# Kernel optimization log

Hardware: AMD Instinct MI355X
Metric: run time of the kernel (lower is better)

The kernel has to match this reference:

```python
import jax, jax.numpy as jnp
import numpy as np
from functools import partial

D_MODEL = 1024
D_HIDDEN = 4096
N_BLOCKS = 4
D_VOCAB = 32000
BATCH = 2
SEQ = 2048
LN_EPS = 1e-5
LRELU_SLOPE = 0.01  # torch nn.LeakyReLU default


def setup_inputs() -> dict:
    key = jax.random.key(0)
    ks = jax.random.split(key, 16)
    d, h, L, v = D_MODEL, D_HIDDEN, N_BLOCKS, D_VOCAB
    scale = d ** 0.5
    inp = {
        "tokens": jax.random.randint(ks[0], (BATCH, SEQ), 0, v, dtype=jnp.int64)
                  if jax.config.jax_enable_x64 else
                  jax.random.randint(ks[0], (BATCH, SEQ), 0, v, dtype=jnp.int32),
        "emb": jax.random.normal(ks[1], (v, d), jnp.float32) * 0.02,
        # per-block stacked params (leading axis = layer) for lax.scan
        "qk": jax.random.normal(ks[2], (L, d, d), jnp.float32) / scale,
        "ov": jax.random.normal(ks[3], (L, d, d), jnp.float32) / scale,
        "w_up": jax.random.normal(ks[4], (L, d, h), jnp.float32) / scale,
        "b_up": jnp.zeros((L, h), jnp.float32),
        "w_hid": jax.random.normal(ks[5], (L, h, h), jnp.float32) / (h ** 0.5),
        "b_hid": jnp.zeros((L, h), jnp.float32),
        "w_down": jax.random.normal(ks[6], (L, h, d), jnp.float32) / (h ** 0.5),
        "b_down": jnp.zeros((L, d), jnp.float32),
        "ln1_g": jnp.ones((L, d), jnp.float32),
        "ln1_b": jnp.zeros((L, d), jnp.float32),
        "ln2_g": jnp.ones((L, d), jnp.float32),
        "ln2_b": jnp.zeros((L, d), jnp.float32),
    }
    return inp


def _layer_norm(x, g, b):
    mu = jnp.mean(x, axis=-1, keepdims=True)
    var = jnp.mean(jnp.square(x - mu), axis=-1, keepdims=True)
    return (x - mu) * jax.lax.rsqrt(var + LN_EPS) * g + b


def _forward(tokens, emb, qk, ov, w_up, b_up, w_hid, b_hid, w_down, b_down,
             ln1_g, ln1_b, ln2_g, ln2_b):
    x = emb[tokens]                                   # [B, S, D]
    seq = tokens.shape[1]
    scale = jnp.asarray(D_MODEL ** 0.5, x.dtype)
    causal = jnp.tril(jnp.ones((seq, seq), bool))     # True = keep

    def block(x, p):
        (qk, ov, w_up, b_up, w_hid, b_hid, w_down, b_down,
         g1, b1, g2, b2) = p
        h = _layer_norm(x, g1, b1)
        # attention: (h @ qk @ h^T) / sqrt(d), causal mask, softmax, @ h @ ov
        scores = jnp.einsum('bsd,de,bte->bst', h, qk, h) / scale
        scores = jnp.where(causal, scores, -jnp.inf)
        attn = jax.nn.softmax(scores, axis=-1)
        x = x + jnp.einsum('bst,btd,de->bse', attn, h, ov)
        # MLP with LeakyReLU after every layer (incl. output)
        m = _layer_norm(x, g2, b2)
        m = jax.nn.leaky_relu(m @ w_up + b_up, LRELU_SLOPE)
        m = jax.nn.leaky_relu(m @ w_hid + b_hid, LRELU_SLOPE)
        m = jax.nn.leaky_relu(m @ w_down + b_down, LRELU_SLOPE)
        return x + m, None

    params = (qk, ov, w_up, b_up, w_hid, b_hid, w_down, b_down,
              ln1_g, ln1_b, ln2_g, ln2_b)
    x, _ = jax.lax.scan(block, x, params)
    return x @ emb.T                                  # [B, S, V] logits


@jax.jit
def reference(tokens, emb, qk, ov, w_up, b_up, w_hid, b_hid, w_down, b_down,
              ln1_g, ln1_b, ln2_g, ln2_b):
    return _forward(tokens, emb, qk, ov, w_up, b_up, w_hid, b_hid,
                    w_down, b_down, ln1_g, ln1_b, ln2_g, ln2_b)
```

## Files before the change

kernel.cpp:

```cpp
#include <hip/hip_runtime.h>

#define BS   4096
#define SEQL 2048
#define DM   1024
#define DH   4096
#define NV   32000

using u16 = unsigned short;

typedef __attribute__((ext_vector_type(8))) short bf16x8;
typedef __attribute__((ext_vector_type(4))) float f32x4;

__device__ __forceinline__ u16 f2b(float f) {
  union { float f; unsigned u; } c; c.f = f;
  unsigned u = c.u;
  u = (u + 0x7FFFu + ((u >> 16) & 1u)) >> 16;
  return (u16)u;
}

__device__ __forceinline__ void gld16(const u16* g, u16* l) {
  __builtin_amdgcn_global_load_lds(
      (__attribute__((address_space(1))) void*)(void*)const_cast<u16*>(g),
      (__attribute__((address_space(3))) void*)l, 16, 0, 0);
}

__global__ __launch_bounds__(256) void k_embed(const int* __restrict__ tok,
                                               const float* __restrict__ emb,
                                               float* __restrict__ x) {
  const long row = blockIdx.x;
  const long e = tok[row];
  ((float4*)(x + row * DM))[threadIdx.x] = ((const float4*)(emb + e * DM))[threadIdx.x];
}

__global__ __launch_bounds__(256) void k_cvt(const float* __restrict__ in,
                                             u16* __restrict__ out, int n4) {
  int i = blockIdx.x * 256 + threadIdx.x;
  if (i < n4) {
    float4 v = ((const float4*)in)[i];
    ushort4 o;
    o.x = f2b(v.x); o.y = f2b(v.y); o.z = f2b(v.z); o.w = f2b(v.w);
    ((ushort4*)out)[i] = o;
  }
}

__global__ __launch_bounds__(256) void k_ln(const float* __restrict__ x,
                                            const float* __restrict__ g,
                                            const float* __restrict__ b,
                                            u16* __restrict__ out) {
  const long row = blockIdx.x;
  const int t = threadIdx.x;
  float4 v = ((const float4*)(x + row * DM))[t];
  float s  = v.x + v.y + v.z + v.w;
  float q2 = v.x*v.x + v.y*v.y + v.z*v.z + v.w*v.w;
#pragma unroll
  for (int o = 1; o < 64; o <<= 1) { s += __shfl_xor(s, o); q2 += __shfl_xor(q2, o); }
  __shared__ float rs_[4], rq_[4];
  const int lane = t & 63, wid = t >> 6;
  if (lane == 0) { rs_[wid] = s; rq_[wid] = q2; }
  __syncthreads();
  s  = rs_[0] + rs_[1] + rs_[2] + rs_[3];
  q2 = rq_[0] + rq_[1] + rq_[2] + rq_[3];
  const float mu   = s * (1.f / 1024.f);
  const float var  = q2 * (1.f / 1024.f) - mu * mu;
  const float rstd = rsqrtf(var + 1e-5f);
  float4 gg = ((const float4*)g)[t];
  float4 bb = ((const float4*)b)[t];
  ushort4 o;
  o.x = f2b((v.x - mu) * rstd * gg.x + bb.x);
  o.y = f2b((v.y - mu) * rstd * gg.y + bb.y);
  o.z = f2b((v.z - mu) * rstd * gg.z + bb.z);
  o.w = f2b((v.w - mu) * rstd * gg.w + bb.w);
  ((ushort4*)(out + row * DM))[t] = o;
}

__device__ __forceinline__ u16 to_b16(float v) { return f2b(v); }
__device__ __forceinline__ u16 to_b16(u16 v)   { return v; }

template <typename T>
__global__ __launch_bounds__(256) void k_transpose64(const T* __restrict__ in,
                                                     u16* __restrict__ out,
                                                     int R, int C, long inz, long outz) {
  __shared__ u16 tile[64][65];
  const T* ip = in + (long)blockIdx.z * inz;
  u16* op = out + (long)blockIdx.z * outz;
  const int tx = threadIdx.x & 63, ty = threadIdx.x >> 6;
  const long c0 = (long)blockIdx.x * 64, r0 = (long)blockIdx.y * 64;
#pragma unroll
  for (int i = 0; i < 16; ++i)
    tile[ty + i * 4][tx] = to_b16(ip[(r0 + ty + i * 4) * C + c0 + tx]);
  __syncthreads();
#pragma unroll
  for (int i = 0; i < 16; ++i)
    op[(c0 + ty + i * 4) * R + r0 + tx] = tile[tx][ty + i * 4];
}

__global__ __launch_bounds__(256) void k_softmax(const float* __restrict__ sc,
                                                 u16* __restrict__ at) {
  const int r = blockIdx.x;
  const long z = blockIdx.y;
  const int t = threadIdx.x;
  const float* row = sc + (z * SEQL + r) * SEQL;
  u16* orow = at + (z * SEQL + r) * SEQL;
  const int ni = (r >> 8) + 1;
  float vals[8];
  float mx = -3.4e38f;
  for (int i = 0; i < ni; ++i) {
    int c = i * 256 + t;
    float v = (c <= r) ? row[c] : -3.4e38f;
    vals[i] = v;
    mx = fmaxf(mx, v);
  }
#pragma unroll
  for (int o = 1; o < 64; o <<= 1) mx = fmaxf(mx, __shfl_xor(mx, o));
  __shared__ float rm[4], rsum[4];
  const int lane = t & 63, wid = t >> 6;
  if (lane == 0) rm[wid] = mx;
  __syncthreads();
  mx = fmaxf(fmaxf(rm[0], rm[1]), fmaxf(rm[2], rm[3]));
  float sum = 0.f;
  for (int i = 0; i < ni; ++i) {
    int c = i * 256 + t;
    float e = (c <= r) ? __expf(vals[i] - mx) : 0.f;
    vals[i] = e;
    sum += e;
  }
#pragma unroll
  for (int o = 1; o < 64; o <<= 1) sum += __shfl_xor(sum, o);
  if (lane == 0) rsum[wid] = sum;
  __syncthreads();
  sum = rsum[0] + rsum[1] + rsum[2] + rsum[3];
  const float inv = 1.f / sum;
  for (int i = 0; i < ni; ++i) orow[i * 256 + t] = f2b(vals[i] * inv);
}

template <int EPI, bool BIAS, bool LRELU, int CAUSAL, bool XOUT>
__global__ __launch_bounds__(256, 2) void k_gemm_bt(
    const u16* __restrict__ A, const u16* __restrict__ B, void* __restrict__ C,
    const float* __restrict__ bias, u16* __restrict__ xb, int K, int N,
    long sAz, long sBz, long sCz, float scale) {
  __shared__ u16 lA[128 * 32];
  __shared__ u16 lB[128 * 32];
  const int t = threadIdx.x;
  const long z = blockIdx.z;
  const long row0 = (long)blockIdx.x * 128;
  const long col0 = (long)blockIdx.y * 128;
  if (CAUSAL == 1 && col0 > row0 + 127) return;
  const int Klim = (CAUSAL == 2) ? min(K, (int)row0 + 128) : K;
  const u16* Ab = A + z * sAz;
  const u16* Bb = B + z * sBz;

  const int rr = t >> 2;
  const int c8 = (t & 3) * 8;
  const u16* gA0 = Ab + (row0 + rr) * K + c8;
  const u16* gA1 = Ab + (row0 + 64 + rr) * K + c8;
  const u16* gB0 = Bb + (col0 + rr) * K + c8;
  const u16* gB1 = Bb + (col0 + 64 + rr) * K + c8;
  u16* sA0 = &lA[rr * 32 + c8];
  u16* sA1 = &lA[(64 + rr) * 32 + c8];
  u16* sB0 = &lB[rr * 32 + c8];
  u16* sB1 = &lB[(64 + rr) * 32 + c8];

  const int lane = t & 63;
  const int w = t >> 6;
  const int wr = (w >> 1) * 64, wc = (w & 1) * 64;
  const int fr = lane & 15;
  const int fk = (lane >> 4) * 8;

  f32x4 acc[4][4] = {};

  for (int k0 = 0; k0 < Klim; k0 += 32) {
    gld16(gA0 + k0, sA0);
    gld16(gA1 + k0, sA1);
    gld16(gB0 + k0, sB0);
    gld16(gB1 + k0, sB1);
    __syncthreads();
    bf16x8 av[4], bv[4];
#pragma unroll
    for (int m = 0; m < 4; ++m) av[m] = *(const bf16x8*)&lA[(wr + m * 16 + fr) * 32 + fk];
#pragma unroll
    for (int n = 0; n < 4; ++n) bv[n] = *(const bf16x8*)&lB[(wc + n * 16 + fr) * 32 + fk];
#pragma unroll
    for (int m = 0; m < 4; ++m)
#pragma unroll
      for (int n = 0; n < 4; ++n)
        acc[m][n] = __builtin_amdgcn_mfma_f32_16x16x32_bf16(av[m], bv[n], acc[m][n], 0, 0, 0);
    __syncthreads();
  }

  const int er = (lane >> 4) * 4;
  const int ec = lane & 15;
#pragma unroll
  for (int m = 0; m < 4; ++m) {
#pragma unroll
    for (int n = 0; n < 4; ++n) {
#pragma unroll
      for (int j = 0; j < 4; ++j) {
        long r = row0 + wr + m * 16 + er + j;
        long c = col0 + wc + n * 16 + ec;
        float v = acc[m][n][j] * scale;
        if (BIAS)  v += bias[c];
        if (LRELU) v = v > 0.f ? v : 0.01f * v;
        long idx = z * sCz + r * (long)N + c;
        if (EPI == 0)      ((float*)C)[idx] = v;
        else if (EPI == 1) ((u16*)C)[idx] = f2b(v);
        else {
          float nv = ((float*)C)[idx] + v;
          ((float*)C)[idx] = nv;
          if (XOUT) xb[idx] = f2b(nv);
        }
      }
    }
  }
}

template <int EPI, bool BIAS, bool LRELU, bool BAR2>
__device__ __forceinline__ void g256_body(
    u16* S, const u16* __restrict__ A, const u16* __restrict__ B,
    void* __restrict__ C, const float* __restrict__ bias, int K, int N, float scale) {
  char* Sc = (char*)S;
  const int t = threadIdx.x;
  const int lane = t & 63;
  const int w = t >> 6;
  const int wr = w >> 2;
  const int wc = w & 3;
  const long row0 = (long)blockIdx.x * 256;
  const long col0 = (long)blockIdx.y * 256;
  const int nt = K >> 6;

  int srow[2], scol[2], ldsb[2];
#pragma unroll
  for (int i = 0; i < 2; ++i) {
    int d = t * 16 + i * 8192;
    int dx = d ^ (((d >> 7) & 3) << 4);
    srow[i] = dx >> 6;
    scol[i] = (dx & 63) >> 1;
    ldsb[i] = d;
  }
  const u16* Abase = A + row0 * (long)K;
  const u16* Bbase = B + col0 * (long)K;

  auto stage = [&](int opb, int kh, int buf, int kb) {
#pragma unroll
    for (int i = 0; i < 2; ++i) {
      const u16* src = (opb ? Bbase : Abase) + (long)srow[i] * K + kb + kh * 32 + scol[i];
      u16* dst = &S[(buf * 4 + opb * 2 + kh) * 8192 + (ldsb[i] >> 1)];
      gld16(src, dst);
    }
  };

  const int fr = lane & 15;
  const int fky = lane >> 4;
  const int axor = ((fr >> 1) & 3) << 4;
  int aoff[8], boff[4];
#pragma unroll
  for (int m = 0; m < 8; ++m)
    aoff[m] = (((wr * 128 + m * 16 + fr) * 64) + fky * 16) ^ axor;
#pragma unroll
  for (int n = 0; n < 4; ++n)
    boff[n] = (((wc * 64 + n * 16 + fr) * 64) + fky * 16) ^ axor;

  f32x4 acc[8][4] = {};
  bf16x8 aA0, aA1, aA2, aA3, aB0, aB1, aB2, aB3;
  bf16x8 bX0, bX1, bX2, bX3, bY0, bY1, bY2, bY3;

#define RD_A(d0, d1, d2, d3, bb, kh, mh)                                   \
  { const char* Ah_ = Sc + (bb) * 65536 + (kh) * 16384;                    \
    d0 = *(const bf16x8*)(Ah_ + aoff[(mh) * 4 + 0]);                       \
    d1 = *(const bf16x8*)(Ah_ + aoff[(mh) * 4 + 1]);                       \
    d2 = *(const bf16x8*)(Ah_ + aoff[(mh) * 4 + 2]);                       \
    d3 = *(const bf16x8*)(Ah_ + aoff[(mh) * 4 + 3]); }
#define RD_B(d0, d1, d2, d3, bb, kh)                                       \
  { const char* Bh_ = Sc + (bb) * 65536 + 32768 + (kh) * 16384;            \
    d0 = *(const bf16x8*)(Bh_ + boff[0]);                                  \
    d1 = *(const bf16x8*)(Bh_ + boff[1]);                                  \
    d2 = *(const bf16x8*)(Bh_ + boff[2]);                                  \
    d3 = *(const bf16x8*)(Bh_ + boff[3]); }
#define MF16(a0, a1, a2, a3, b0, b1, b2, b3, mh)                                                     \
  __builtin_amdgcn_s_setprio(1);                                                                     \
  acc[(mh)*4+0][0] = __builtin_amdgcn_mfma_f32_16x16x32_bf16(a0, b0, acc[(mh)*4+0][0], 0, 0, 0);     \
  acc[(mh)*4+0][1] = __builtin_amdgcn_mfma_f32_16x16x32_bf16(a0, b1, acc[(mh)*4+0][1], 0, 0, 0);     \
  acc[(mh)*4+0][2] = __builtin_amdgcn_mfma_f32_16x16x32_bf16(a0, b2, acc[(mh)*4+0][2], 0, 0, 0);     \
  acc[(mh)*4+0][3] = __builtin_amdgcn_mfma_f32_16x16x32_bf16(a0, b3, acc[(mh)*4+0][3], 0, 0, 0);     \
  acc[(mh)*4+1][0] = __builtin_amdgcn_mfma_f32_16x16x32_bf16(a1, b0, acc[(mh)*4+1][0], 0, 0, 0);     \
  acc[(mh)*4+1][1] = __builtin_amdgcn_mfma_f32_16x16x32_bf16(a1, b1, acc[(mh)*4+1][1], 0, 0, 0);     \
  acc[(mh)*4+1][2] = __builtin_amdgcn_mfma_f32_16x16x32_bf16(a1, b2, acc[(mh)*4+1][2], 0, 0, 0);     \
  acc[(mh)*4+1][3] = __builtin_amdgcn_mfma_f32_16x16x32_bf16(a1, b3, acc[(mh)*4+1][3], 0, 0, 0);     \
  acc[(mh)*4+2][0] = __builtin_amdgcn_mfma_f32_16x16x32_bf16(a2, b0, acc[(mh)*4+2][0], 0, 0, 0);     \
  acc[(mh)*4+2][1] = __builtin_amdgcn_mfma_f32_16x16x32_bf16(a2, b1, acc[(mh)*4+2][1], 0, 0, 0);     \
  acc[(mh)*4+2][2] = __builtin_amdgcn_mfma_f32_16x16x32_bf16(a2, b2, acc[(mh)*4+2][2], 0, 0, 0);     \
  acc[(mh)*4+2][3] = __builtin_amdgcn_mfma_f32_16x16x32_bf16(a2, b3, acc[(mh)*4+2][3], 0, 0, 0);     \
  acc[(mh)*4+3][0] = __builtin_amdgcn_mfma_f32_16x16x32_bf16(a3, b0, acc[(mh)*4+3][0], 0, 0, 0);     \
  acc[(mh)*4+3][1] = __builtin_amdgcn_mfma_f32_16x16x32_bf16(a3, b1, acc[(mh)*4+3][1], 0, 0, 0);     \
  acc[(mh)*4+3][2] = __builtin_amdgcn_mfma_f32_16x16x32_bf16(a3, b2, acc[(mh)*4+3][2], 0, 0, 0);     \
  acc[(mh)*4+3][3] = __builtin_amdgcn_mfma_f32_16x16x32_bf16(a3, b3, acc[(mh)*4+3][3], 0, 0, 0);     \
  __builtin_amdgcn_s_setprio(0);

  stage(0, 0, 0, 0);
  stage(1, 0, 0, 0);
  stage(0, 1, 0, 0);
  stage(1, 1, 0, 0);
  asm volatile("s_waitcnt vmcnt(4)" ::: "memory");
  __builtin_amdgcn_s_barrier();
  RD_A(aA0, aA1, aA2, aA3, 0, 0, 0);
  RD_B(bX0, bX1, bX2, bX3, 0, 0);

  int cur = 0;
  for (int tt = 0; tt < nt; ++tt) {
    const int knext = (tt + 1 < nt ? tt + 1 : tt) * 64;
    const int nx = cur ^ 1;
    RD_A(aB0, aB1, aB2, aB3, cur, 0, 1);
    stage(0, 0, nx, knext);
    if (BAR2) __builtin_amdgcn_s_barrier();
    MF16(aA0, aA1, aA2, aA3, bX0, bX1, bX2, bX3, 0);
    asm volatile("s_waitcnt vmcnt(2)" ::: "memory");
    __builtin_amdgcn_s_barrier();
    RD_A(aA0, aA1, aA2, aA3, cur, 1, 0);
    RD_B(bY0, bY1, bY2, bY3, cur, 1);
    stage(1, 0, nx, knext);
    if (BAR2) __builtin_amdgcn_s_barrier();
    MF16(aB0, aB1, aB2, aB3, bX0, bX1, bX2, bX3, 1);
    __builtin_amdgcn_s_barrier();
    RD_A(aB0, aB1, aB2, aB3, cur, 1, 1);
    stage(0, 1, nx, knext);
    if (BAR2) __builtin_amdgcn_s_barrier();
    MF16(aA0, aA1, aA2, aA3, bY0, bY1, bY2, bY3, 0);
    asm volatile("s_waitcnt vmcnt(2)" ::: "memory");
    __builtin_amdgcn_s_barrier();
    RD_A(aA0, aA1, aA2, aA3, nx, 0, 0);
    RD_B(bX0, bX1, bX2, bX3, nx, 0);
    stage(1, 1, nx, knext);
    if (BAR2) __builtin_amdgcn_s_barrier();
    MF16(aB0, aB1, aB2, aB3, bY0, bY1, bY2, bY3, 1);
    __builtin_amdgcn_s_barrier();
    cur = nx;
  }
  asm volatile("s_waitcnt vmcnt(0)" ::: "memory");
#undef RD_A
#undef RD_B
#undef MF16

  const int er = (lane >> 4) * 4;
  const int ec = lane & 15;
#pragma unroll
  for (int m = 0; m < 8; ++m) {
#pragma unroll
    for (int n = 0; n < 4; ++n) {
#pragma unroll
      for (int j = 0; j < 4; ++j) {
        long r = row0 + wr * 128 + m * 16 + er + j;
        long c = col0 + wc * 64 + n * 16 + ec;
        float v = acc[m][n][j] * scale;
        if (BIAS)  v += bias[c];
        if (LRELU) v = v > 0.f ? v : 0.01f * v;
        if (EPI == 0)      ((float*)C)[r * (long)N + c] = v;
        else if (EPI == 1) ((u16*)C)[r * (long)N + c] = f2b(v);
        else               ((float*)C)[r * (long)N + c] += v;
      }
    }
  }
}

__global__ __launch_bounds__(512, 1) void k_g256_up(
    const u16* __restrict__ A, const u16* __restrict__ B, void* __restrict__ C,
    const float* __restrict__ bias, int K, int N, float scale) {
  __shared__ u16 S[65536];
  g256_body<1, true, true, false>(S, A, B, C, bias, K, N, scale);
}
__global__ __launch_bounds__(512, 1) void k_g256_hid(
    const u16* __restrict__ A, const u16* __restrict__ B, void* __restrict__ C,
    const float* __restrict__ bias, int K, int N, float scale) {
  __shared__ u16 S[65536];
  g256_body<1, true, true, true>(S, A, B, C, bias, K, N, scale);
}
__global__ __launch_bounds__(512, 1) void k_g256_log(
    const u16* __restrict__ A, const u16* __restrict__ B, void* __restrict__ C,
    const float* __restrict__ bias, int K, int N, float scale) {
  __shared__ u16 S[65536];
  g256_body<0, false, false, false>(S, A, B, C, bias, K, N, scale);
}

extern "C" void kernel_launch(void* const* d_in, const int* in_sizes, int n_in,
                              void* d_out, int out_size, void* d_ws, size_t ws_size,
                              hipStream_t stream) {
  const int*   tokens = (const int*)d_in[0];
  const float* emb    = (const float*)d_in[1];
  const float* qk     = (const float*)d_in[2];
  const float* ov     = (const float*)d_in[3];
  const float* wup    = (const float*)d_in[4];
  const float* bup    = (const float*)d_in[5];
  const float* whid   = (const float*)d_in[6];
  const float* bhid   = (const float*)d_in[7];
  const float* wdown  = (const float*)d_in[8];
  const float* bdown  = (const float*)d_in[9];
  const float* g1     = (const float*)d_in[10];
  const float* b1     = (const float*)d_in[11];
  const float* g2     = (const float*)d_in[12];
  const float* b2     = (const float*)d_in[13];

  char* Ob = (char*)d_out;
  float* scores = (float*)(Ob + 0);
  u16*   attn   = (u16*)(Ob + 33554432);
  u16*   m1     = (u16*)(Ob + 50331648);
  u16*   m2     = (u16*)(Ob + 83886080);
  u16*   qkT    = (u16*)(Ob + 117440512);
  u16*   ovT    = (u16*)(Ob + 125829120);
  u16*   upT    = (u16*)(Ob + 134217728);
  u16*   hidT   = (u16*)(Ob + 167772160);
  u16*   downT  = (u16*)(Ob + 301989888);
  float* xres   = (float*)(Ob + 335544320);
  u16*   h      = (u16*)(Ob + 352321536);
  u16*   hT     = (u16*)(Ob + 360710144);
  u16*   q      = (u16*)(Ob + 369098752);
  u16*   attnV  = (u16*)(Ob + 377487360);

  u16* embB = (u16*)d_ws;
  u16* xB   = (u16*)((char*)d_ws + 65536000);

  k_embed<<<dim3(BS), 256, 0, stream>>>(tokens, emb, xres);
  k_cvt<<<dim3(32000), 256, 0, stream>>>(emb, embB, 8192000);

  k_transpose64<float><<<dim3(16, 16, 4), 256, 0, stream>>>(qk,    qkT,   1024, 1024, 1048576,  1048576);
  k_transpose64<float><<<dim3(16, 16, 4), 256, 0, stream>>>(ov,    ovT,   1024, 1024, 1048576,  1048576);
  k_transpose64<float><<<dim3(64, 16, 4), 256, 0, stream>>>(wup,   upT,   1024, 4096, 4194304,  4194304);
  k_transpose64<float><<<dim3(64, 64, 4), 256, 0, stream>>>(whid,  hidT,  4096, 4096, 16777216, 16777216);
  k_transpose64<float><<<dim3(16, 64, 4), 256, 0, stream>>>(wdown, downT, 4096, 1024, 4194304,  4194304);

  for (int l = 0; l < 4; ++l) {
    k_ln<<<dim3(BS), 256, 0, stream>>>(xres, g1 + l * 1024, b1 + l * 1024, h);
    k_transpose64<u16><<<dim3(16, 32, 2), 256, 0, stream>>>(h, hT, 2048, 1024, 2048L * 1024, 1024L * 2048);
    k_gemm_bt<1, false, false, 0, false><<<dim3(32, 8, 1), 256, 0, stream>>>(
        h, qkT + (long)l * 1048576, q, nullptr, nullptr, 1024, 1024, 0, 0, 0, 0.03125f);
    k_gemm_bt<0, false, false, 1, false><<<dim3(16, 16, 2), 256, 0, stream>>>(
        q, h, scores, nullptr, nullptr, 1024, 2048, 2048L * 1024, 2048L * 1024, 2048L * 2048, 1.f);
    k_softmax<<<dim3(2048, 2), 256, 0, stream>>>(scores, attn);
    k_gemm_bt<1, false, false, 2, false><<<dim3(16, 8, 2), 256, 0, stream>>>(
        attn, hT, attnV, nullptr, nullptr, 2048, 1024, 2048L * 2048, 1024L * 2048, 2048L * 1024, 1.f);
    k_gemm_bt<2, false, false, 0, false><<<dim3(32, 8, 1), 256, 0, stream>>>(
        attnV, ovT + (long)l * 1048576, xres, nullptr, nullptr, 1024, 1024, 0, 0, 0, 1.f);

    k_ln<<<dim3(BS), 256, 0, stream>>>(xres, g2 + l * 1024, b2 + l * 1024, h);
    k_g256_up<<<dim3(16, 16), 512, 0, stream>>>(
        h, upT + (long)l * 4194304, m1, bup + l * 4096, 1024, 4096, 1.f);
    k_g256_hid<<<dim3(16, 16), 512, 0, stream>>>(
        m1, hidT + (long)l * 16777216, m2, bhid + l * 4096, 4096, 4096, 1.f);
    if (l == 3) {
      k_gemm_bt<2, true, true, 0, true><<<dim3(32, 8, 1), 256, 0, stream>>>(
          m2, downT + (long)l * 4194304, xres, bdown + l * 1024, xB, 4096, 1024, 0, 0, 0, 1.f);
    } else {
      k_gemm_bt<2, true, true, 0, false><<<dim3(32, 8, 1), 256, 0, stream>>>(
          m2, downT + (long)l * 4194304, xres, bdown + l * 1024, nullptr, 4096, 1024, 0, 0, 0, 1.f);
    }
  }

  k_g256_log<<<dim3(16, 125), 512, 0, stream>>>(
      xB, embB, (float*)d_out, nullptr, 1024, 32000, 1.f);
}
```

Measured before the change: 2.152 ms.

## Restructure 256-tile GEMM main loop to single A register set with explicit LDS waits

The main loop of the 256x256 GEMM body no longer double-buffers A fragments in registers. It now reads A (and B) fragments right before each MFMA group, adds an explicit lgkmcnt(0) wait with a scheduling barrier, and always uses the extra barrier that was previously only on for the hidden GEMM. This cuts register pressure and makes LDS read timing deterministic. In exchange, LDS read latency is exposed before each MFMA block instead of being hidden behind the previous block's compute, and the vmcnt wait points move.

```diff
diff --git a/kernel.cpp b/kernel.cpp
--- a/kernel.cpp
+++ b/kernel.cpp
@@ -213,7 +213,7 @@
   }
 }
 
-template <int EPI, bool BIAS, bool LRELU, bool BAR2>
+template <int EPI, bool BIAS, bool LRELU>
 __device__ __forceinline__ void g256_body(
     u16* S, const u16* __restrict__ A, const u16* __restrict__ B,
     void* __restrict__ C, const float* __restrict__ bias, int K, int N, float scale) {
@@ -260,39 +260,42 @@
     boff[n] = (((wc * 64 + n * 16 + fr) * 64) + fky * 16) ^ axor;
 
   f32x4 acc[8][4] = {};
-  bf16x8 aA0, aA1, aA2, aA3, aB0, aB1, aB2, aB3;
+  bf16x8 av0, av1, av2, av3;
   bf16x8 bX0, bX1, bX2, bX3, bY0, bY1, bY2, bY3;
 
-#define RD_A(d0, d1, d2, d3, bb, kh, mh)                                   \
+#define RD_A(bb, kh, mh)                                                   \
   { const char* Ah_ = Sc + (bb) * 65536 + (kh) * 16384;                    \
-    d0 = *(const bf16x8*)(Ah_ + aoff[(mh) * 4 + 0]);                       \
-    d1 = *(const bf16x8*)(Ah_ + aoff[(mh) * 4 + 1]);                       \
-    d2 = *(const bf16x8*)(Ah_ + aoff[(mh) * 4 + 2]);                       \
-    d3 = *(const bf16x8*)(Ah_ + aoff[(mh) * 4 + 3]); }
+    av0 = *(const bf16x8*)(Ah_ + aoff[(mh) * 4 + 0]);                      \
+    av1 = *(const bf16x8*)(Ah_ + aoff[(mh) * 4 + 1]);                      \
+    av2 = *(const bf16x8*)(Ah_ + aoff[(mh) * 4 + 2]);                      \
+    av3 = *(const bf16x8*)(Ah_ + aoff[(mh) * 4 + 3]); }
 #define RD_B(d0, d1, d2, d3, bb, kh)                                       \
   { const char* Bh_ = Sc + (bb) * 65536 + 32768 + (kh) * 16384;            \
     d0 = *(const bf16x8*)(Bh_ + boff[0]);                                  \
     d1 = *(const bf16x8*)(Bh_ + boff[1]);                                  \
     d2 = *(const bf16x8*)(Bh_ + boff[2]);                                  \
     d3 = *(const bf16x8*)(Bh_ + boff[3]); }
-#define MF16(a0, a1, a2, a3, b0, b1, b2, b3, mh)                                                     \
+#define WAIT_LGKM()                                                        \
+  asm volatile("s_waitcnt lgkmcnt(0)" ::: "memory");                       \
+  __builtin_amdgcn_sched_barrier(0);
+#define MF16(b0, b1, b2, b3, mh)                                                                     \
   __builtin_amdgcn_s_setprio(1);                                                                     \
-  acc[(mh)*4+0][0] = __builtin_amdgcn_mfma_f32_16x16x32_bf16(a0, b0, acc[(mh)*4+0][0], 0, 0, 0);     \
-  acc[(mh)*4+0][1] = __builtin_amdgcn_mfma_f32_16x16x32_bf16(a0, b1, acc[(mh)*4+0][1], 0, 0, 0);     \
-  acc[(mh)*4+0][2] = __builtin_amdgcn_mfma_f32_16x16x32_bf16(a0, b2, acc[(mh)*4+0][2], 0, 0, 0);     \
-  acc[(mh)*4+0][3] = __builtin_amdgcn_mfma_f32_16x16x32_bf16(a0, b3, acc[(mh)*4+0][3], 0, 0, 0);     \
-  acc[(mh)*4+1][0] = __builtin_amdgcn_mfma_f32_16x16x32_bf16(a1, b0, acc[(mh)*4+1][0], 0, 0, 0);     \
-  acc[(mh)*4+1][1] = __builtin_amdgcn_mfma_f32_16x16x32_bf16(a1, b1, acc[(mh)*4+1][1], 0, 0, 0);     \
-  acc[(mh)*4+1][2] = __builtin_amdgcn_mfma_f32_16x16x32_bf16(a1, b2, acc[(mh)*4+1][2], 0, 0, 0);     \
-  acc[(mh)*4+1][3] = __builtin_amdgcn_mfma_f32_16x16x32_bf16(a1, b3, acc[(mh)*4+1][3], 0, 0, 0);     \
-  acc[(mh)*4+2][0] = __builtin_amdgcn_mfma_f32_16x16x32_bf16(a2, b0, acc[(mh)*4+2][0], 0, 0, 0);     \
-  acc[(mh)*4+2][1] = __builtin_amdgcn_mfma_f32_16x16x32_bf16(a2, b1, acc[(mh)*4+2][1], 0, 0, 0);     \
-  acc[(mh)*4+2][2] = __builtin_amdgcn_mfma_f32_16x16x32_bf16(a2, b2, acc[(mh)*4+2][2], 0, 0, 0);     \
-  acc[(mh)*4+2][3] = __builtin_amdgcn_mfma_f32_16x16x32_bf16(a2, b3, acc[(mh)*4+2][3], 0, 0, 0);     \
-  acc[(mh)*4+3][0] = __builtin_amdgcn_mfma_f32_16x16x32_bf16(a3, b0, acc[(mh)*4+3][0], 0, 0, 0);     \
-  acc[(mh)*4+3][1] = __builtin_amdgcn_mfma_f32_16x16x32_bf16(a3, b1, acc[(mh)*4+3][1], 0, 0, 0);     \
-  acc[(mh)*4+3][2] = __builtin_amdgcn_mfma_f32_16x16x32_bf16(a3, b2, acc[(mh)*4+3][2], 0, 0, 0);     \
-  acc[(mh)*4+3][3] = __builtin_amdgcn_mfma_f32_16x16x32_bf16(a3, b3, acc[(mh)*4+3][3], 0, 0, 0);     \
+  acc[(mh)*4+0][0] = __builtin_amdgcn_mfma_f32_16x16x32_bf16(av0, b0, acc[(mh)*4+0][0], 0, 0, 0);    \
+  acc[(mh)*4+0][1] = __builtin_amdgcn_mfma_f32_16x16x32_bf16(av0, b1, acc[(mh)*4+0][1], 0, 0, 0);    \
+  acc[(mh)*4+0][2] = __builtin_amdgcn_mfma_f32_16x16x32_bf16(av0, b2, acc[(mh)*4+0][2], 0, 0, 0);    \
+  acc[(mh)*4+0][3] = __builtin_amdgcn_mfma_f32_16x16x32_bf16(av0, b3, acc[(mh)*4+0][3], 0, 0, 0);    \
+  acc[(mh)*4+1][0] = __builtin_amdgcn_mfma_f32_16x16x32_bf16(av1, b0, acc[(mh)*4+1][0], 0, 0, 0);    \
+  acc[(mh)*4+1][1] = __builtin_amdgcn_mfma_f32_16x16x32_bf16(av1, b1, acc[(mh)*4+1][1], 0, 0, 0);    \
+  acc[(mh)*4+1][2] = __builtin_amdgcn_mfma_f32_16x16x32_bf16(av1, b2, acc[(mh)*4+1][2], 0, 0, 0);    \
+  acc[(mh)*4+1][3] = __builtin_amdgcn_mfma_f32_16x16x32_bf16(av1, b3, acc[(mh)*4+1][3], 0, 0, 0);    \
+  acc[(mh)*4+2][0] = __builtin_amdgcn_mfma_f32_16x16x32_bf16(av2, b0, acc[(mh)*4+2][0], 0, 0, 0);    \
+  acc[(mh)*4+2][1] = __builtin_amdgcn_mfma_f32_16x16x32_bf16(av2, b1, acc[(mh)*4+2][1], 0, 0, 0);    \
+  acc[(mh)*4+2][2] = __builtin_amdgcn_mfma_f32_16x16x32_bf16(av2, b2, acc[(mh)*4+2][2], 0, 0, 0);    \
+  acc[(mh)*4+2][3] = __builtin_amdgcn_mfma_f32_16x16x32_bf16(av2, b3, acc[(mh)*4+2][3], 0, 0, 0);    \
+  acc[(mh)*4+3][0] = __builtin_amdgcn_mfma_f32_16x16x32_bf16(av3, b0, acc[(mh)*4+3][0], 0, 0, 0);    \
+  acc[(mh)*4+3][1] = __builtin_amdgcn_mfma_f32_16x16x32_bf16(av3, b1, acc[(mh)*4+3][1], 0, 0, 0);    \
+  acc[(mh)*4+3][2] = __builtin_amdgcn_mfma_f32_16x16x32_bf16(av3, b2, acc[(mh)*4+3][2], 0, 0, 0);    \
+  acc[(mh)*4+3][3] = __builtin_amdgcn_mfma_f32_16x16x32_bf16(av3, b3, acc[(mh)*4+3][3], 0, 0, 0);    \
   __builtin_amdgcn_s_setprio(0);
 
   stage(0, 0, 0, 0);
@@ -301,42 +304,45 @@
   stage(1, 1, 0, 0);
   asm volatile("s_waitcnt vmcnt(4)" ::: "memory");
   __builtin_amdgcn_s_barrier();
-  RD_A(aA0, aA1, aA2, aA3, 0, 0, 0);
-  RD_B(bX0, bX1, bX2, bX3, 0, 0);
 
   int cur = 0;
   for (int tt = 0; tt < nt; ++tt) {
     const int knext = (tt + 1 < nt ? tt + 1 : tt) * 64;
     const int nx = cur ^ 1;
-    RD_A(aB0, aB1, aB2, aB3, cur, 0, 1);
+    RD_A(cur, 0, 0);
+    RD_B(bX0, bX1, bX2, bX3, cur, 0);
     stage(0, 0, nx, knext);
-    if (BAR2) __builtin_amdgcn_s_barrier();
-    MF16(aA0, aA1, aA2, aA3, bX0, bX1, bX2, bX3, 0);
-    asm volatile("s_waitcnt vmcnt(2)" ::: "memory");
-    __builtin_amdgcn_s_barrier();
-    RD_A(aA0, aA1, aA2, aA3, cur, 1, 0);
+    __builtin_amdgcn_s_barrier();
+    WAIT_LGKM();
+    MF16(bX0, bX1, bX2, bX3, 0);
+    __builtin_amdgcn_s_barrier();
+    RD_A(cur, 0, 1);
+    stage(1, 0, nx, knext);
+    __builtin_amdgcn_s_barrier();
+    WAIT_LGKM();
+    MF16(bX0, bX1, bX2, bX3, 1);
+    asm volatile("s_waitcnt vmcnt(4)" ::: "memory");
+    __builtin_amdgcn_s_barrier();
+    RD_A(cur, 1, 0);
     RD_B(bY0, bY1, bY2, bY3, cur, 1);
-    stage(1, 0, nx, knext);
-    if (BAR2) __builtin_amdgcn_s_barrier();
-    MF16(aB0, aB1, aB2, aB3, bX0, bX1, bX2, bX3, 1);
-    __builtin_amdgcn_s_barrier();
-    RD_A(aB0, aB1, aB2, aB3, cur, 1, 1);
     stage(0, 1, nx, knext);
-    if (BAR2) __builtin_amdgcn_s_barrier();
-    MF16(aA0, aA1, aA2, aA3, bY0, bY1, bY2, bY3, 0);
-    asm volatile("s_waitcnt vmcnt(2)" ::: "memory");
-    __builtin_amdgcn_s_barrier();
-    RD_A(aA0, aA1, aA2, aA3, nx, 0, 0);
-    RD_B(bX0, bX1, bX2, bX3, nx, 0);
+    __builtin_amdgcn_s_barrier();
+    WAIT_LGKM();
+    MF16(bY0, bY1, bY2, bY3, 0);
+    __builtin_amdgcn_s_barrier();
+    RD_A(cur, 1, 1);
     stage(1, 1, nx, knext);
-    if (BAR2) __builtin_amdgcn_s_barrier();
-    MF16(aB0, aB1, aB2, aB3, bY0, bY1, bY2, bY3, 1);
+    __builtin_amdgcn_s_barrier();
+    WAIT_LGKM();
+    MF16(bY0, bY1, bY2, bY3, 1);
+    asm volatile("s_waitcnt vmcnt(4)" ::: "memory");
     __builtin_amdgcn_s_barrier();
     cur = nx;
   }
   asm volatile("s_waitcnt vmcnt(0)" ::: "memory");
 #undef RD_A
 #undef RD_B
+#undef WAIT_LGKM
 #undef MF16
 
   const int er = (lane >> 4) * 4;
@@ -364,19 +370,19 @@
     const u16* __restrict__ A, const u16* __restrict__ B, void* __restrict__ C,
     const float* __restrict__ bias, int K, int N, float scale) {
   __shared__ u16 S[65536];
-  g256_body<1, true, true, false>(S, A, B, C, bias, K, N, scale);
+  g256_body<1, true, true>(S, A, B, C, bias, K, N, scale);
 }
 __global__ __launch_bounds__(512, 1) void k_g256_hid(
     const u16* __restrict__ A, const u16* __restrict__ B, void* __restrict__ C,
     const float* __restrict__ bias, int K, int N, float scale) {
   __shared__ u16 S[65536];
-  g256_body<1, true, true, true>(S, A, B, C, bias, K, N, scale);
+  g256_body<1, true, true>(S, A, B, C, bias, K, N, scale);
 }
 __global__ __launch_bounds__(512, 1) void k_g256_log(
     const u16* __restrict__ A, const u16* __restrict__ B, void* __restrict__ C,
     const float* __restrict__ bias, int K, int N, float scale) {
   __shared__ u16 S[65536];
-  g256_body<0, false, false, false>(S, A, B, C, bias, K, N, scale);
+  g256_body<0, false, false>(S, A, B, C, bias, K, N, scale);
 }
 
 extern "C" void kernel_launch(void* const* d_in, const int* in_sizes, int n_in,
```

New measurement: 2.142 ms, median of 2. Within noise of the previous version (-0.5%).
